# Performance work log

Measured on AMD Instinct MI355X. Metric: run time of the kernel, lower is better.

## Reference

```python
import jax, jax.numpy as jnp
import numpy as np

B, N, K = 4, 8192, 32
HID, INP = 64, 64
IN_CH = HID + INP  # 128; SetConv fc1 sees IN_CH + 3 (relative pos)


def setup_inputs() -> dict:
    key = jax.random.key(0)
    ks = jax.random.split(key, 10)
    return {
        "h": jax.random.normal(ks[0], (B, N, HID), jnp.float32),
        "x": jax.random.normal(ks[1], (B, N, INP), jnp.float32),
        "c": jax.random.normal(ks[2], (B, N, 3), jnp.float32),
        "W1": jax.random.normal(ks[3], (3, IN_CH + 3, HID), jnp.float32) * 0.05,
        "b1": jnp.zeros((3, HID), jnp.float32),
        "W2": jax.random.normal(ks[4], (3, HID, HID), jnp.float32) * 0.05,
        "b2": jnp.zeros((3, HID), jnp.float32),
        "W3": jax.random.normal(ks[5], (3, HID, HID), jnp.float32) * 0.05,
        "b3": jnp.zeros((3, HID), jnp.float32),
        "neigh_idx": jax.random.randint(ks[6], (B, N, K), 0, N, jnp.int32),
        "edge_feats": jax.random.normal(ks[7], (B, N, K, 3), jnp.float32),
    }


def reference(h, x, c, W1, b1, W2, b2, W3, b3, neigh_idx, edge_feats):
    # c (point coordinates) is unused by the GRU body, matching the torch source.
    slope = 0.1

    def setconv(i, feat):
        # gather K neighbor features per point: [B, N, K, C]
        g = jax.vmap(lambda fb, ib: fb[ib])(feat, neigh_idx)
        e = jnp.concatenate([g, edge_feats], axis=-1)  # [B, N, K, C+3]
        y = jax.nn.leaky_relu(jnp.einsum('bnkc,cd->bnkd', e, W1[i]) + b1[i], slope)
        y = y.max(axis=2)  # pool over neighbors -> [B, N, HID]
        y = jax.nn.leaky_relu(y @ W2[i] + b2[i], slope)
        return y @ W3[i] + b3[i]

    hx = jnp.concatenate([h, x], axis=2)
    z = jax.nn.sigmoid(setconv(0, hx))
    r = jax.nn.sigmoid(setconv(1, hx))
    q = jnp.tanh(setconv(2, jnp.concatenate([r * h, x], axis=2)))
    return (1.0 - z) * h + z * q
```

## Files before the change

kernel.cpp:

```cpp
#include <hip/hip_runtime.h>
#include <math.h>

typedef unsigned short u16;
typedef unsigned int u32;
typedef __attribute__((ext_vector_type(8))) short s8v;
typedef __attribute__((ext_vector_type(4))) float f4v;

#define KNBR 32
#define MFMA16(a, b, c) __builtin_amdgcn_mfma_f32_16x16x32_bf16((a), (b), (c), 0, 0, 0)

__device__ __forceinline__ float bf2f(u16 u) { return __uint_as_float((u32)u << 16); }
__device__ __forceinline__ float bflo(u32 u) { return __uint_as_float(u << 16); }
__device__ __forceinline__ float bfhi(u32 u) { return __uint_as_float(u & 0xffff0000u); }
__device__ __forceinline__ u16 f2bf(float f) {
    u32 u = __float_as_uint(f);
    return (u16)((u + 0x7fffu + ((u >> 16) & 1u)) >> 16);
}
__device__ __forceinline__ u32 pk2(float a, float b) {
    return (u32)f2bf(a) | ((u32)f2bf(b) << 16);
}
__device__ __forceinline__ float leaky(float v) { return v >= 0.f ? v : 0.1f * v; }
__device__ __forceinline__ float sigm(float v) { return 1.f / (1.f + expf(-v)); }

__device__ __forceinline__ int swz_plb(int b, int full) {
    if (!full) return b << 6;
    int xcd = b & 7;
    int within = ((b >> 3) << 1) | (xcd & 1);
    return ((xcd >> 1) << 13) + (within << 6);
}

#define T2O 8704
#define T3O 13056
#define T4O 17664
#define T5O 22272
#define T6O 24576
#define TTOT 26880

__global__ __launch_bounds__(512) void k_prep(
    const float* __restrict__ W1f, const float* __restrict__ W2f,
    const float* __restrict__ W3f, u32* __restrict__ TB)
{
    int id = blockIdx.x * 512 + threadIdx.x;
    if (id >= TTOT) return;
    u32 word = 0;
    if (id < T2O) {
        int g = id / 4352, r = id - g * 4352;
        int n = r / 68, kp = r - n * 68;
        if (kp < 64)
            word = pk2(W1f[g * 8384 + kp * 128 + n], W1f[g * 8384 + kp * 128 + 64 + n]);
    } else if (id < T3O) {
        int r = id - T2O;
        int n = r / 68, kp = r - n * 68;
        if (kp < 64)
            word = pk2(W1f[16768 + kp * 128 + n], W1f[16768 + kp * 128 + 64 + n]);
    } else if (id < T4O) {
        int r = id - T3O;
        int g = r / 2304, r2 = r - g * 2304;
        int n = r2 / 36, kp = r2 - n * 36;
        if (kp < 32)
            word = pk2(W2f[g * 4096 + kp * 128 + n], W2f[g * 4096 + kp * 128 + 64 + n]);
    } else if (id < T5O) {
        int r = id - T4O;
        int g = r / 2304, r2 = r - g * 2304;
        int n = r2 / 36, kp = r2 - n * 36;
        if (kp < 32)
            word = pk2(W3f[g * 4096 + kp * 128 + n], W3f[g * 4096 + kp * 128 + 64 + n]);
    } else if (id < T6O) {
        int r = id - T5O;
        int n = r / 36, kp = r - n * 36;
        if (kp < 32)
            word = pk2(W2f[8192 + kp * 128 + n], W2f[8192 + kp * 128 + 64 + n]);
    } else {
        int r = id - T6O;
        int n = r / 36, kp = r - n * 36;
        if (kp < 32)
            word = pk2(W3f[8192 + kp * 128 + n], W3f[8192 + kp * 128 + 64 + n]);
    }
    TB[id] = word;
}


__global__ __launch_bounds__(512) void k_gemm_p01(
    const float* __restrict__ h, const float* __restrict__ x,
    const u32* __restrict__ TB, const float* __restrict__ b1f,
    u32* __restrict__ P01, int p0, int full)
{
    __shared__ u32 a_lds[64 * 68];
    __shared__ u32 wb[8704];
    int t = threadIdx.x;
    int plb = swz_plb(blockIdx.x, full);
    int pgb = p0 + plb;
    for (int i = 0; i < 8; ++i) {
        int id = t + i * 512;
        int p = id >> 6, cw = id & 63;
        const float* src = (cw < 32) ? (h + (size_t)(pgb + p) * 64 + cw * 2)
                                     : (x + (size_t)(pgb + p) * 64 + (cw - 32) * 2);
        float2 v = *(const float2*)src;
        a_lds[p * 68 + cw] = pk2(v.x, v.y);
    }
    for (int i = 0; i < 17; ++i) wb[t + i * 512] = TB[t + i * 512];
    __syncthreads();
    int lane = t & 63;
    int w = __builtin_amdgcn_readfirstlane(t >> 6);
    int m = w & 3, npair = w >> 2;
    int quad = lane >> 4, l15 = lane & 15;
    f4v acc[2][2];
    #pragma unroll
    for (int g = 0; g < 2; ++g)
        #pragma unroll
        for (int nt = 0; nt < 2; ++nt) {
            float b = b1f[g * 64 + (npair * 2 + nt) * 16 + l15];
            acc[g][nt] = (f4v){b, b, b, b};
        }
    #pragma unroll
    for (int kb = 0; kb < 4; ++kb) {
        s8v af = *(const s8v*)&a_lds[(m * 16 + l15) * 68 + kb * 16 + quad * 4];
        #pragma unroll
        for (int g = 0; g < 2; ++g)
            #pragma unroll
            for (int nt = 0; nt < 2; ++nt) {
                s8v bf = *(const s8v*)&wb[(g * 64 + (npair * 2 + nt) * 16 + l15) * 68
                                          + kb * 16 + quad * 4];
                acc[g][nt] = MFMA16(af, bf, acc[g][nt]);
            }
    }
    #pragma unroll
    for (int nt = 0; nt < 2; ++nt)
        #pragma unroll
        for (int r = 0; r < 4; ++r) {
            int pt = m * 16 + quad * 4 + r;
            int ch = (npair * 2 + nt) * 16 + l15;
            P01[(size_t)(plb + pt) * 64 + ch] = pk2(acc[0][nt][r], acc[1][nt][r]);
        }
}

__global__ __launch_bounds__(512) void k_fuse01(
    const u32* __restrict__ P01, const float* __restrict__ W1f,
    const u32* __restrict__ TB,
    const int* __restrict__ nidx, const float* __restrict__ ef,
    const float* __restrict__ h, const float* __restrict__ x,
    const float* __restrict__ b1f, const float* __restrict__ b2f,
    const float* __restrict__ b3f,
    u16* __restrict__ Z, float* __restrict__ P2, int p0, int full)
{
    __shared__ u32 a_lds[64 * 68];
    __shared__ u32 wb[4608];
    __shared__ u32 idx_l[1024];
    __shared__ u32 ef_p[2048];
    __shared__ u32 e2_p[1024];
    int t = threadIdx.x;
    int plb = swz_plb(blockIdx.x, full);
    int pg0 = p0 + plb;
    int rbase = ((pg0 >> 13) << 13) - p0;
    int lane = t & 63;
    int w = __builtin_amdgcn_readfirstlane(t >> 6);
    int quad = lane >> 4, l15 = lane & 15;
    u16* y16 = (u16*)a_lds;

    for (int i = 0; i < 9; ++i) wb[t + i * 512] = TB[T3O + t + i * 512];
    for (int i = 0; i < 2; ++i) {
        int id = t + i * 512;
        int pt = id >> 4, k2 = id & 15;
        int2 nn = *(const int2*)(nidx + (size_t)(pg0 + pt) * KNBR + 2 * k2);
        idx_l[id] = (u32)(rbase + nn.x) | ((u32)(rbase + nn.y) << 16);
        const float* e = ef + ((size_t)(pg0 + pt) * KNBR + 2 * k2) * 3;
        float2 a = *(const float2*)(e);
        float2 b = *(const float2*)(e + 2);
        float2 c = *(const float2*)(e + 4);
        uint2 ev; ev.x = pk2(a.x, a.y); ev.y = pk2(b.y, c.x);
        ((uint2*)ef_p)[id] = ev;
        e2_p[id] = pk2(b.x, c.y);
    }
    __syncthreads();
    {
        float w00 = W1f[8192 + lane], w01 = W1f[8256 + lane], w02 = W1f[8320 + lane];
        float w10 = W1f[16576 + lane], w11 = W1f[16640 + lane], w12 = W1f[16704 + lane];
        const u32* P01l = P01 + lane;
        for (int pp = 0; pp < 8; ++pp) {
            int lp = w * 8 + pp;
            const u32* ib2 = &idx_l[lp * 16];
            const uint2* eb2 = (const uint2*)&ef_p[lp * 32];
            const u32* e2b = &e2_p[lp * 16];
            float m0 = -1e30f, m1 = -1e30f;
            #pragma unroll
            for (int k2 = 0; k2 < 16; ++k2) {
                u32 rw = ib2[k2];
                uint2 ew = eb2[k2];
                u32 e2w = e2b[k2];
                u32 g0 = P01l[(rw & 0xffffu) * 64];
                u32 g1 = P01l[(rw >> 16) * 64];
                float e00 = bflo(ew.x), e01 = bfhi(ew.x), e02 = bflo(e2w);
                float e10 = bflo(ew.y), e11 = bfhi(ew.y), e12 = bfhi(e2w);
                m0 = fmaxf(m0, bflo(g0) + e00 * w00 + e01 * w01 + e02 * w02);
                m1 = fmaxf(m1, bfhi(g0) + e00 * w10 + e01 * w11 + e02 * w12);
                m0 = fmaxf(m0, bflo(g1) + e10 * w00 + e11 * w01 + e12 * w02);
                m1 = fmaxf(m1, bfhi(g1) + e10 * w10 + e11 * w11 + e12 * w12);
            }
            y16[lp * 136 + lane]      = f2bf(leaky(m0));
            y16[lp * 136 + 64 + lane] = f2bf(leaky(m1));
        }
    }
    __syncthreads();
    int m = w & 3, g = w >> 2;
    f4v acc[4];
    #pragma unroll
    for (int nt = 0; nt < 4; ++nt) {
        float b = b2f[g * 64 + nt * 16 + l15];
        acc[nt] = (f4v){b, b, b, b};
    }
    #pragma unroll
    for (int kb = 0; kb < 2; ++kb) {
        s8v af = *(const s8v*)&a_lds[(m * 16 + l15) * 68 + g * 32 + kb * 16 + quad * 4];
        #pragma unroll
        for (int nt = 0; nt < 4; ++nt) {
            s8v bf = *(const s8v*)&wb[(g * 64 + nt * 16 + l15) * 36 + kb * 16 + quad * 4];
            acc[nt] = MFMA16(af, bf, acc[nt]);
        }
    }
    #pragma unroll
    for (int nt = 0; nt < 4; ++nt)
        #pragma unroll
        for (int r = 0; r < 4; ++r)
            y16[(m * 16 + quad * 4 + r) * 136 + g * 64 + nt * 16 + l15] =
                f2bf(leaky(acc[nt][r]));
    __syncthreads();
    for (int i = 0; i < 9; ++i) wb[t + i * 512] = TB[T4O + t + i * 512];
    __syncthreads();
    #pragma unroll
    for (int nt = 0; nt < 4; ++nt) {
        float b = b3f[g * 64 + nt * 16 + l15];
        acc[nt] = (f4v){b, b, b, b};
    }
    #pragma unroll
    for (int kb = 0; kb < 2; ++kb) {
        s8v af = *(const s8v*)&a_lds[(m * 16 + l15) * 68 + g * 32 + kb * 16 + quad * 4];
        #pragma unroll
        for (int nt = 0; nt < 4; ++nt) {
            s8v bf = *(const s8v*)&wb[(g * 64 + nt * 16 + l15) * 36 + kb * 16 + quad * 4];
            acc[nt] = MFMA16(af, bf, acc[nt]);
        }
    }
    __syncthreads();
    if (g == 0) {
        #pragma unroll
        for (int nt = 0; nt < 4; ++nt)
            #pragma unroll
            for (int r = 0; r < 4; ++r) {
                int pt = m * 16 + quad * 4 + r;
                int ch = nt * 16 + l15;
                Z[(size_t)(plb + pt) * 64 + ch] = f2bf(sigm(acc[nt][r]));
            }
    } else {
        #pragma unroll
        for (int nt = 0; nt < 4; ++nt)
            #pragma unroll
            for (int r = 0; r < 4; ++r) {
                int pt = m * 16 + quad * 4 + r;
                int ch = nt * 16 + l15;
                float hv = h[(size_t)(pg0 + pt) * 64 + ch];
                y16[pt * 136 + ch] = f2bf(sigm(acc[nt][r]) * hv);
            }
    }
    for (int i = 0; i < 4; ++i) {
        int id = t + i * 512;
        int p = id >> 5, cw = id & 31;
        float2 v = *(const float2*)(x + (size_t)(pg0 + p) * 64 + cw * 2);
        a_lds[p * 68 + 32 + cw] = pk2(v.x, v.y);
    }
    for (int i = 0; i < 9; ++i) {
        int id = t + i * 512;
        if (id < 4352) wb[id] = TB[T2O + id];
    }
    __syncthreads();
    int nh = w >> 2;
    f4v pacc[2];
    #pragma unroll
    for (int nt = 0; nt < 2; ++nt) {
        float b = b1f[128 + (nh * 2 + nt) * 16 + l15];
        pacc[nt] = (f4v){b, b, b, b};
    }
    #pragma unroll
    for (int kb = 0; kb < 4; ++kb) {
        s8v af = *(const s8v*)&a_lds[(m * 16 + l15) * 68 + kb * 16 + quad * 4];
        #pragma unroll
        for (int nt = 0; nt < 2; ++nt) {
            s8v bf = *(const s8v*)&wb[((nh * 2 + nt) * 16 + l15) * 68 + kb * 16 + quad * 4];
            pacc[nt] = MFMA16(af, bf, pacc[nt]);
        }
    }
    #pragma unroll
    for (int nt = 0; nt < 2; ++nt)
        #pragma unroll
        for (int r = 0; r < 4; ++r) {
            int pt = m * 16 + quad * 4 + r;
            int ch = (nh * 2 + nt) * 16 + l15;
            P2[(size_t)(plb + pt) * 64 + ch] = pacc[nt][r];
        }
}

__global__ __launch_bounds__(512) void k_fuse2(
    const float* __restrict__ P2, const float* __restrict__ W1f,
    const u32* __restrict__ TB,
    const int* __restrict__ nidx, const float* __restrict__ ef,
    const float* __restrict__ b2f, const float* __restrict__ b3f,
    const float* __restrict__ h, const u16* __restrict__ Z,
    float* __restrict__ out, int p0, int full)
{
    __shared__ u32 a_lds[64 * 36];
    __shared__ u32 wb[2304];
    __shared__ u32 idx_l[1024];
    __shared__ u32 ef_p[2048];
    __shared__ u32 e2_p[1024];
    int t = threadIdx.x;
    int plb = swz_plb(blockIdx.x, full);
    int pg0 = p0 + plb;
    int rbase = ((pg0 >> 13) << 13) - p0;
    int lane = t & 63;
    int w = __builtin_amdgcn_readfirstlane(t >> 6);
    int quad = lane >> 4, l15 = lane & 15;
    u16* y16 = (u16*)a_lds;

    for (int i = 0; i < 5; ++i) {
        int id = t + i * 512;
        if (id < 2304) wb[id] = TB[T5O + id];
    }
    for (int i = 0; i < 2; ++i) {
        int id = t + i * 512;
        int pt = id >> 4, k2 = id & 15;
        int2 nn = *(const int2*)(nidx + (size_t)(pg0 + pt) * KNBR + 2 * k2);
        idx_l[id] = (u32)(rbase + nn.x) | ((u32)(rbase + nn.y) << 16);
        const float* e = ef + ((size_t)(pg0 + pt) * KNBR + 2 * k2) * 3;
        float2 a = *(const float2*)(e);
        float2 b = *(const float2*)(e + 2);
        float2 c = *(const float2*)(e + 4);
        uint2 ev; ev.x = pk2(a.x, a.y); ev.y = pk2(b.y, c.x);
        ((uint2*)ef_p)[id] = ev;
        e2_p[id] = pk2(b.x, c.y);
    }
    __syncthreads();
    {
        const float* W = W1f + 2 * 8384;
        float w0 = W[8192 + lane], w1 = W[8256 + lane], w2 = W[8320 + lane];
        const float* P2l = P2 + lane;
        for (int pp = 0; pp < 8; ++pp) {
            int lp = w * 8 + pp;
            const u32* ib2 = &idx_l[lp * 16];
            const uint2* eb2 = (const uint2*)&ef_p[lp * 32];
            const u32* e2b = &e2_p[lp * 16];
            float m = -1e30f;
            #pragma unroll
            for (int k2 = 0; k2 < 16; ++k2) {
                u32 rw = ib2[k2];
                uint2 ew = eb2[k2];
                u32 e2w = e2b[k2];
                float g0 = P2l[(rw & 0xffffu) * 64];
                float g1 = P2l[(rw >> 16) * 64];
                float e00 = bflo(ew.x), e01 = bfhi(ew.x), e02 = bflo(e2w);
                float e10 = bflo(ew.y), e11 = bfhi(ew.y), e12 = bfhi(e2w);
                m = fmaxf(m, g0 + e00 * w0 + e01 * w1 + e02 * w2);
                m = fmaxf(m, g1 + e10 * w0 + e11 * w1 + e12 * w2);
            }
            y16[lp * 72 + lane] = f2bf(leaky(m));
        }
    }
    __syncthreads();
    int m = w & 3, nh = w >> 2;
    f4v acc[2];
    #pragma unroll
    for (int nt = 0; nt < 2; ++nt) {
        float b = b2f[128 + (nh * 2 + nt) * 16 + l15];
        acc[nt] = (f4v){b, b, b, b};
    }
    #pragma unroll
    for (int kb = 0; kb < 2; ++kb) {
        s8v af = *(const s8v*)&a_lds[(m * 16 + l15) * 36 + kb * 16 + quad * 4];
        #pragma unroll
        for (int nt = 0; nt < 2; ++nt) {
            s8v bf = *(const s8v*)&wb[((nh * 2 + nt) * 16 + l15) * 36 + kb * 16 + quad * 4];
            acc[nt] = MFMA16(af, bf, acc[nt]);
        }
    }
    __syncthreads();
    #pragma unroll
    for (int nt = 0; nt < 2; ++nt)
        #pragma unroll
        for (int r = 0; r < 4; ++r)
            y16[(m * 16 + quad * 4 + r) * 72 + (nh * 2 + nt) * 16 + l15] =
                f2bf(leaky(acc[nt][r]));
    for (int i = 0; i < 5; ++i) {
        int id = t + i * 512;
        if (id < 2304) wb[id] = TB[T6O + id];
    }
    __syncthreads();
    #pragma unroll
    for (int nt = 0; nt < 2; ++nt) {
        float b = b3f[128 + (nh * 2 + nt) * 16 + l15];
        acc[nt] = (f4v){b, b, b, b};
    }
    #pragma unroll
    for (int kb = 0; kb < 2; ++kb) {
        s8v af = *(const s8v*)&a_lds[(m * 16 + l15) * 36 + kb * 16 + quad * 4];
        #pragma unroll
        for (int nt = 0; nt < 2; ++nt) {
            s8v bf = *(const s8v*)&wb[((nh * 2 + nt) * 16 + l15) * 36 + kb * 16 + quad * 4];
            acc[nt] = MFMA16(af, bf, acc[nt]);
        }
    }
    #pragma unroll
    for (int nt = 0; nt < 2; ++nt)
        #pragma unroll
        for (int r = 0; r < 4; ++r) {
            int pt = m * 16 + quad * 4 + r;
            int ch = (nh * 2 + nt) * 16 + l15;
            int pl = plb + pt;
            int pg = p0 + pl;
            float z = bf2f(Z[(size_t)pl * 64 + ch]);
            float hv = h[(size_t)pg * 64 + ch];
            out[(size_t)pg * 64 + ch] = (1.f - z) * hv + z * tanhf(acc[nt][r]);
        }
}

extern "C" void kernel_launch(void* const* d_in, const int* in_sizes, int n_in,
                              void* d_out, int out_size, void* d_ws, size_t ws_size,
                              hipStream_t stream)
{
    const float* h  = (const float*)d_in[0];
    const float* x  = (const float*)d_in[1];
    const float* W1 = (const float*)d_in[3];
    const float* b1 = (const float*)d_in[4];
    const float* W2 = (const float*)d_in[5];
    const float* b2 = (const float*)d_in[6];
    const float* W3 = (const float*)d_in[7];
    const float* b3 = (const float*)d_in[8];
    const int* nidx = (const int*)d_in[9];
    const float* ef = (const float*)d_in[10];
    float* out = (float*)d_out;

    char* wsb = (char*)d_ws;
    size_t need_full = 32768ull * 640ull + (size_t)TTOT * 4ull;
    size_t PN = (ws_size >= need_full) ? 32768 : 8192;
    int passes = (int)(32768 / PN);
    int full = (PN == 32768) ? 1 : 0;

    u32* P01  = (u32*)wsb;
    u16* Z    = (u16*)(wsb + PN * 256);
    float* P2 = (float*)(wsb + PN * 384);
    u32* TB   = (u32*)(wsb + PN * 640);

    k_prep<<<dim3((TTOT + 511) / 512), 512, 0, stream>>>(W1, W2, W3, TB);
    for (int s = 0; s < passes; ++s) {
        int p0 = (int)(s * PN);
        dim3 g((unsigned)(PN / 64));
        k_gemm_p01<<<g, 512, 0, stream>>>(h, x, TB, b1, P01, p0, full);
        k_fuse01  <<<g, 512, 0, stream>>>(P01, W1, TB, nidx, ef, h, x,
                                          b1, b2, b3, Z, P2, p0, full);
        k_fuse2   <<<g, 512, 0, stream>>>(P2, W1, TB, nidx, ef,
                                          b2, b3, h, Z, out, p0, full);
    }
}
```

Baseline: 164.3 us.

## Precompute packed edge data once and double block threads to 1024

```diff
diff --git a/kernel.cpp b/kernel.cpp
--- a/kernel.cpp
+++ b/kernel.cpp
@@ -79,8 +79,28 @@
     TB[id] = word;
 }
 
-
-__global__ __launch_bounds__(512) void k_gemm_p01(
+__global__ __launch_bounds__(256) void k_prep_edges(
+    const int* __restrict__ nidx, const float* __restrict__ ef,
+    u32* __restrict__ EP, int p0, int full)
+{
+    int tid = blockIdx.x * 256 + threadIdx.x;
+    int ptl = tid >> 4, k2 = tid & 15;
+    int ptg = p0 + ptl;
+    int2 nn = *(const int2*)(nidx + (size_t)ptg * KNBR + 2 * k2);
+    int rb = full ? ((ptg >> 13) << 13) : 0;
+    u32 idxw = (u32)(rb + nn.x) | ((u32)(rb + nn.y) << 16);
+    const float* e = ef + ((size_t)ptg * KNBR + 2 * k2) * 3;
+    float2 a = *(const float2*)(e);
+    float2 b = *(const float2*)(e + 2);
+    float2 c = *(const float2*)(e + 4);
+    u32* row = EP + (size_t)ptl * 64;
+    row[k2] = idxw;
+    ((uint2*)(row + 16))[k2] = make_uint2(pk2(a.x, a.y), pk2(b.y, c.x));
+    row[48 + k2] = pk2(b.x, c.y);
+}
+
+
+__global__ __launch_bounds__(1024) void k_gemm_p01(
     const float* __restrict__ h, const float* __restrict__ x,
     const u32* __restrict__ TB, const float* __restrict__ b1f,
     u32* __restrict__ P01, int p0, int full)
@@ -90,54 +110,48 @@
     int t = threadIdx.x;
     int plb = swz_plb(blockIdx.x, full);
     int pgb = p0 + plb;
-    for (int i = 0; i < 8; ++i) {
-        int id = t + i * 512;
+    for (int i = 0; i < 4; ++i) {
+        int id = t + i * 1024;
         int p = id >> 6, cw = id & 63;
         const float* src = (cw < 32) ? (h + (size_t)(pgb + p) * 64 + cw * 2)
                                      : (x + (size_t)(pgb + p) * 64 + (cw - 32) * 2);
         float2 v = *(const float2*)src;
         a_lds[p * 68 + cw] = pk2(v.x, v.y);
     }
-    for (int i = 0; i < 17; ++i) wb[t + i * 512] = TB[t + i * 512];
+    for (int i = 0; i < 9; ++i) {
+        int id = t + i * 1024;
+        if (id < 8704) wb[id] = TB[id];
+    }
     __syncthreads();
     int lane = t & 63;
     int w = __builtin_amdgcn_readfirstlane(t >> 6);
-    int m = w & 3, npair = w >> 2;
+    int m = w & 3, nt = w >> 2;
     int quad = lane >> 4, l15 = lane & 15;
-    f4v acc[2][2];
-    #pragma unroll
-    for (int g = 0; g < 2; ++g)
-        #pragma unroll
-        for (int nt = 0; nt < 2; ++nt) {
-            float b = b1f[g * 64 + (npair * 2 + nt) * 16 + l15];
-            acc[g][nt] = (f4v){b, b, b, b};
-        }
+    f4v acc0, acc1;
+    {
+        float b0 = b1f[nt * 16 + l15];
+        float b1 = b1f[64 + nt * 16 + l15];
+        acc0 = (f4v){b0, b0, b0, b0};
+        acc1 = (f4v){b1, b1, b1, b1};
+    }
     #pragma unroll
     for (int kb = 0; kb < 4; ++kb) {
         s8v af = *(const s8v*)&a_lds[(m * 16 + l15) * 68 + kb * 16 + quad * 4];
-        #pragma unroll
-        for (int g = 0; g < 2; ++g)
-            #pragma unroll
-            for (int nt = 0; nt < 2; ++nt) {
-                s8v bf = *(const s8v*)&wb[(g * 64 + (npair * 2 + nt) * 16 + l15) * 68
-                                          + kb * 16 + quad * 4];
-                acc[g][nt] = MFMA16(af, bf, acc[g][nt]);
-            }
-    }
-    #pragma unroll
-    for (int nt = 0; nt < 2; ++nt)
-        #pragma unroll
-        for (int r = 0; r < 4; ++r) {
-            int pt = m * 16 + quad * 4 + r;
-            int ch = (npair * 2 + nt) * 16 + l15;
-            P01[(size_t)(plb + pt) * 64 + ch] = pk2(acc[0][nt][r], acc[1][nt][r]);
-        }
-}
-
-__global__ __launch_bounds__(512) void k_fuse01(
+        s8v bf0 = *(const s8v*)&wb[(nt * 16 + l15) * 68 + kb * 16 + quad * 4];
+        s8v bf1 = *(const s8v*)&wb[(64 + nt * 16 + l15) * 68 + kb * 16 + quad * 4];
+        acc0 = MFMA16(af, bf0, acc0);
+        acc1 = MFMA16(af, bf1, acc1);
+    }
+    #pragma unroll
+    for (int r = 0; r < 4; ++r) {
+        int pt = m * 16 + quad * 4 + r;
+        P01[(size_t)(plb + pt) * 64 + nt * 16 + l15] = pk2(acc0[r], acc1[r]);
+    }
+}
+
+__global__ __launch_bounds__(1024) void k_fuse01(
     const u32* __restrict__ P01, const float* __restrict__ W1f,
-    const u32* __restrict__ TB,
-    const int* __restrict__ nidx, const float* __restrict__ ef,
+    const u32* __restrict__ TB, const u32* __restrict__ EP,
     const float* __restrict__ h, const float* __restrict__ x,
     const float* __restrict__ b1f, const float* __restrict__ b2f,
     const float* __restrict__ b3f,
@@ -145,48 +159,37 @@
 {
     __shared__ u32 a_lds[64 * 68];
     __shared__ u32 wb[4608];
-    __shared__ u32 idx_l[1024];
-    __shared__ u32 ef_p[2048];
-    __shared__ u32 e2_p[1024];
+    __shared__ u32 ep_l[64 * 64];
     int t = threadIdx.x;
     int plb = swz_plb(blockIdx.x, full);
     int pg0 = p0 + plb;
-    int rbase = ((pg0 >> 13) << 13) - p0;
     int lane = t & 63;
     int w = __builtin_amdgcn_readfirstlane(t >> 6);
     int quad = lane >> 4, l15 = lane & 15;
     u16* y16 = (u16*)a_lds;
 
-    for (int i = 0; i < 9; ++i) wb[t + i * 512] = TB[T3O + t + i * 512];
-    for (int i = 0; i < 2; ++i) {
-        int id = t + i * 512;
-        int pt = id >> 4, k2 = id & 15;
-        int2 nn = *(const int2*)(nidx + (size_t)(pg0 + pt) * KNBR + 2 * k2);
-        idx_l[id] = (u32)(rbase + nn.x) | ((u32)(rbase + nn.y) << 16);
-        const float* e = ef + ((size_t)(pg0 + pt) * KNBR + 2 * k2) * 3;
-        float2 a = *(const float2*)(e);
-        float2 b = *(const float2*)(e + 2);
-        float2 c = *(const float2*)(e + 4);
-        uint2 ev; ev.x = pk2(a.x, a.y); ev.y = pk2(b.y, c.x);
-        ((uint2*)ef_p)[id] = ev;
-        e2_p[id] = pk2(b.x, c.y);
+    for (int i = 0; i < 5; ++i) {
+        int id = t + i * 1024;
+        if (id < 4608) wb[id] = TB[T3O + id];
+    }
+    for (int i = 0; i < 4; ++i) {
+        int id = t + i * 1024;
+        ep_l[id] = EP[(size_t)plb * 64 + id];
     }
     __syncthreads();
     {
         float w00 = W1f[8192 + lane], w01 = W1f[8256 + lane], w02 = W1f[8320 + lane];
         float w10 = W1f[16576 + lane], w11 = W1f[16640 + lane], w12 = W1f[16704 + lane];
         const u32* P01l = P01 + lane;
-        for (int pp = 0; pp < 8; ++pp) {
-            int lp = w * 8 + pp;
-            const u32* ib2 = &idx_l[lp * 16];
-            const uint2* eb2 = (const uint2*)&ef_p[lp * 32];
-            const u32* e2b = &e2_p[lp * 16];
+        for (int pp = 0; pp < 4; ++pp) {
+            int lp = w * 4 + pp;
+            const u32* ib = &ep_l[lp * 64];
             float m0 = -1e30f, m1 = -1e30f;
             #pragma unroll
             for (int k2 = 0; k2 < 16; ++k2) {
-                u32 rw = ib2[k2];
-                uint2 ew = eb2[k2];
-                u32 e2w = e2b[k2];
+                u32 rw = ib[k2];
+                uint2 ew = ((const uint2*)(ib + 16))[k2];
+                u32 e2w = ib[48 + k2];
                 u32 g0 = P01l[(rw & 0xffffu) * 64];
                 u32 g1 = P01l[(rw >> 16) * 64];
                 float e00 = bflo(ew.x), e01 = bfhi(ew.x), e02 = bflo(e2w);
@@ -201,158 +204,141 @@
         }
     }
     __syncthreads();
-    int m = w & 3, g = w >> 2;
-    f4v acc[4];
-    #pragma unroll
-    for (int nt = 0; nt < 4; ++nt) {
-        float b = b2f[g * 64 + nt * 16 + l15];
+    int m = w & 3, c = w >> 2, g = c >> 1, np = c & 1;
+    f4v acc[2];
+    #pragma unroll
+    for (int nt = 0; nt < 2; ++nt) {
+        float b = b2f[g * 64 + (np * 2 + nt) * 16 + l15];
         acc[nt] = (f4v){b, b, b, b};
     }
     #pragma unroll
     for (int kb = 0; kb < 2; ++kb) {
         s8v af = *(const s8v*)&a_lds[(m * 16 + l15) * 68 + g * 32 + kb * 16 + quad * 4];
         #pragma unroll
-        for (int nt = 0; nt < 4; ++nt) {
-            s8v bf = *(const s8v*)&wb[(g * 64 + nt * 16 + l15) * 36 + kb * 16 + quad * 4];
+        for (int nt = 0; nt < 2; ++nt) {
+            s8v bf = *(const s8v*)&wb[(g * 64 + (np * 2 + nt) * 16 + l15) * 36
+                                      + kb * 16 + quad * 4];
             acc[nt] = MFMA16(af, bf, acc[nt]);
         }
     }
-    #pragma unroll
-    for (int nt = 0; nt < 4; ++nt)
+    __syncthreads();
+    #pragma unroll
+    for (int nt = 0; nt < 2; ++nt)
         #pragma unroll
         for (int r = 0; r < 4; ++r)
-            y16[(m * 16 + quad * 4 + r) * 136 + g * 64 + nt * 16 + l15] =
+            y16[(m * 16 + quad * 4 + r) * 136 + g * 64 + (np * 2 + nt) * 16 + l15] =
                 f2bf(leaky(acc[nt][r]));
-    __syncthreads();
-    for (int i = 0; i < 9; ++i) wb[t + i * 512] = TB[T4O + t + i * 512];
-    __syncthreads();
-    #pragma unroll
-    for (int nt = 0; nt < 4; ++nt) {
-        float b = b3f[g * 64 + nt * 16 + l15];
+    for (int i = 0; i < 5; ++i) {
+        int id = t + i * 1024;
+        if (id < 4608) wb[id] = TB[T4O + id];
+    }
+    __syncthreads();
+    #pragma unroll
+    for (int nt = 0; nt < 2; ++nt) {
+        float b = b3f[g * 64 + (np * 2 + nt) * 16 + l15];
         acc[nt] = (f4v){b, b, b, b};
     }
     #pragma unroll
     for (int kb = 0; kb < 2; ++kb) {
         s8v af = *(const s8v*)&a_lds[(m * 16 + l15) * 68 + g * 32 + kb * 16 + quad * 4];
         #pragma unroll
-        for (int nt = 0; nt < 4; ++nt) {
-            s8v bf = *(const s8v*)&wb[(g * 64 + nt * 16 + l15) * 36 + kb * 16 + quad * 4];
+        for (int nt = 0; nt < 2; ++nt) {
+            s8v bf = *(const s8v*)&wb[(g * 64 + (np * 2 + nt) * 16 + l15) * 36
+                                      + kb * 16 + quad * 4];
             acc[nt] = MFMA16(af, bf, acc[nt]);
         }
     }
     __syncthreads();
     if (g == 0) {
         #pragma unroll
-        for (int nt = 0; nt < 4; ++nt)
+        for (int nt = 0; nt < 2; ++nt)
             #pragma unroll
             for (int r = 0; r < 4; ++r) {
                 int pt = m * 16 + quad * 4 + r;
-                int ch = nt * 16 + l15;
+                int ch = (np * 2 + nt) * 16 + l15;
                 Z[(size_t)(plb + pt) * 64 + ch] = f2bf(sigm(acc[nt][r]));
             }
     } else {
         #pragma unroll
-        for (int nt = 0; nt < 4; ++nt)
+        for (int nt = 0; nt < 2; ++nt)
             #pragma unroll
             for (int r = 0; r < 4; ++r) {
                 int pt = m * 16 + quad * 4 + r;
-                int ch = nt * 16 + l15;
+                int ch = (np * 2 + nt) * 16 + l15;
                 float hv = h[(size_t)(pg0 + pt) * 64 + ch];
                 y16[pt * 136 + ch] = f2bf(sigm(acc[nt][r]) * hv);
             }
     }
-    for (int i = 0; i < 4; ++i) {
-        int id = t + i * 512;
+    for (int i = 0; i < 2; ++i) {
+        int id = t + i * 1024;
         int p = id >> 5, cw = id & 31;
         float2 v = *(const float2*)(x + (size_t)(pg0 + p) * 64 + cw * 2);
         a_lds[p * 68 + 32 + cw] = pk2(v.x, v.y);
     }
-    for (int i = 0; i < 9; ++i) {
-        int id = t + i * 512;
+    for (int i = 0; i < 5; ++i) {
+        int id = t + i * 1024;
         if (id < 4352) wb[id] = TB[T2O + id];
     }
     __syncthreads();
-    int nh = w >> 2;
-    f4v pacc[2];
-    #pragma unroll
-    for (int nt = 0; nt < 2; ++nt) {
-        float b = b1f[128 + (nh * 2 + nt) * 16 + l15];
-        pacc[nt] = (f4v){b, b, b, b};
+    int n = w >> 2;
+    f4v pacc;
+    {
+        float b = b1f[128 + n * 16 + l15];
+        pacc = (f4v){b, b, b, b};
     }
     #pragma unroll
     for (int kb = 0; kb < 4; ++kb) {
         s8v af = *(const s8v*)&a_lds[(m * 16 + l15) * 68 + kb * 16 + quad * 4];
-        #pragma unroll
-        for (int nt = 0; nt < 2; ++nt) {
-            s8v bf = *(const s8v*)&wb[((nh * 2 + nt) * 16 + l15) * 68 + kb * 16 + quad * 4];
-            pacc[nt] = MFMA16(af, bf, pacc[nt]);
-        }
-    }
-    #pragma unroll
-    for (int nt = 0; nt < 2; ++nt)
-        #pragma unroll
-        for (int r = 0; r < 4; ++r) {
-            int pt = m * 16 + quad * 4 + r;
-            int ch = (nh * 2 + nt) * 16 + l15;
-            P2[(size_t)(plb + pt) * 64 + ch] = pacc[nt][r];
-        }
-}
-
-__global__ __launch_bounds__(512) void k_fuse2(
+        s8v bf = *(const s8v*)&wb[(n * 16 + l15) * 68 + kb * 16 + quad * 4];
+        pacc = MFMA16(af, bf, pacc);
+    }
+    #pragma unroll
+    for (int r = 0; r < 4; ++r) {
+        int pt = m * 16 + quad * 4 + r;
+        P2[(size_t)(plb + pt) * 64 + n * 16 + l15] = pacc[r];
+    }
+}
+
+__global__ __launch_bounds__(1024) void k_fuse2(
     const float* __restrict__ P2, const float* __restrict__ W1f,
-    const u32* __restrict__ TB,
-    const int* __restrict__ nidx, const float* __restrict__ ef,
+    const u32* __restrict__ TB, const u32* __restrict__ EP,
     const float* __restrict__ b2f, const float* __restrict__ b3f,
     const float* __restrict__ h, const u16* __restrict__ Z,
     float* __restrict__ out, int p0, int full)
 {
     __shared__ u32 a_lds[64 * 36];
     __shared__ u32 wb[2304];
-    __shared__ u32 idx_l[1024];
-    __shared__ u32 ef_p[2048];
-    __shared__ u32 e2_p[1024];
+    __shared__ u32 ep_l[64 * 64];
     int t = threadIdx.x;
     int plb = swz_plb(blockIdx.x, full);
     int pg0 = p0 + plb;
-    int rbase = ((pg0 >> 13) << 13) - p0;
     int lane = t & 63;
     int w = __builtin_amdgcn_readfirstlane(t >> 6);
     int quad = lane >> 4, l15 = lane & 15;
     u16* y16 = (u16*)a_lds;
 
-    for (int i = 0; i < 5; ++i) {
-        int id = t + i * 512;
+    for (int i = 0; i < 3; ++i) {
+        int id = t + i * 1024;
         if (id < 2304) wb[id] = TB[T5O + id];
     }
-    for (int i = 0; i < 2; ++i) {
-        int id = t + i * 512;
-        int pt = id >> 4, k2 = id & 15;
-        int2 nn = *(const int2*)(nidx + (size_t)(pg0 + pt) * KNBR + 2 * k2);
-        idx_l[id] = (u32)(rbase + nn.x) | ((u32)(rbase + nn.y) << 16);
-        const float* e = ef + ((size_t)(pg0 + pt) * KNBR + 2 * k2) * 3;
-        float2 a = *(const float2*)(e);
-        float2 b = *(const float2*)(e + 2);
-        float2 c = *(const float2*)(e + 4);
-        uint2 ev; ev.x = pk2(a.x, a.y); ev.y = pk2(b.y, c.x);
-        ((uint2*)ef_p)[id] = ev;
-        e2_p[id] = pk2(b.x, c.y);
+    for (int i = 0; i < 4; ++i) {
+        int id = t + i * 1024;
+        ep_l[id] = EP[(size_t)plb * 64 + id];
     }
     __syncthreads();
     {
         const float* W = W1f + 2 * 8384;
         float w0 = W[8192 + lane], w1 = W[8256 + lane], w2 = W[8320 + lane];
         const float* P2l = P2 + lane;
-        for (int pp = 0; pp < 8; ++pp) {
-            int lp = w * 8 + pp;
-            const u32* ib2 = &idx_l[lp * 16];
-            const uint2* eb2 = (const uint2*)&ef_p[lp * 32];
-            const u32* e2b = &e2_p[lp * 16];
+        for (int pp = 0; pp < 4; ++pp) {
+            int lp = w * 4 + pp;
+            const u32* ib = &ep_l[lp * 64];
             float m = -1e30f;
             #pragma unroll
             for (int k2 = 0; k2 < 16; ++k2) {
-                u32 rw = ib2[k2];
-                uint2 ew = eb2[k2];
-                u32 e2w = e2b[k2];
+                u32 rw = ib[k2];
+                uint2 ew = ((const uint2*)(ib + 16))[k2];
+                u32 e2w = ib[48 + k2];
                 float g0 = P2l[(rw & 0xffffu) * 64];
                 float g1 = P2l[(rw >> 16) * 64];
                 float e00 = bflo(ew.x), e01 = bfhi(ew.x), e02 = bflo(e2w);
@@ -364,60 +350,47 @@
         }
     }
     __syncthreads();
-    int m = w & 3, nh = w >> 2;
-    f4v acc[2];
-    #pragma unroll
-    for (int nt = 0; nt < 2; ++nt) {
-        float b = b2f[128 + (nh * 2 + nt) * 16 + l15];
-        acc[nt] = (f4v){b, b, b, b};
+    int m = w & 3, n = w >> 2;
+    f4v acc;
+    {
+        float b = b2f[128 + n * 16 + l15];
+        acc = (f4v){b, b, b, b};
     }
     #pragma unroll
     for (int kb = 0; kb < 2; ++kb) {
         s8v af = *(const s8v*)&a_lds[(m * 16 + l15) * 36 + kb * 16 + quad * 4];
-        #pragma unroll
-        for (int nt = 0; nt < 2; ++nt) {
-            s8v bf = *(const s8v*)&wb[((nh * 2 + nt) * 16 + l15) * 36 + kb * 16 + quad * 4];
-            acc[nt] = MFMA16(af, bf, acc[nt]);
-        }
-    }
-    __syncthreads();
-    #pragma unroll
-    for (int nt = 0; nt < 2; ++nt)
-        #pragma unroll
-        for (int r = 0; r < 4; ++r)
-            y16[(m * 16 + quad * 4 + r) * 72 + (nh * 2 + nt) * 16 + l15] =
-                f2bf(leaky(acc[nt][r]));
-    for (int i = 0; i < 5; ++i) {
-        int id = t + i * 512;
+        s8v bf = *(const s8v*)&wb[(n * 16 + l15) * 36 + kb * 16 + quad * 4];
+        acc = MFMA16(af, bf, acc);
+    }
+    __syncthreads();
+    #pragma unroll
+    for (int r = 0; r < 4; ++r)
+        y16[(m * 16 + quad * 4 + r) * 72 + n * 16 + l15] = f2bf(leaky(acc[r]));
+    for (int i = 0; i < 3; ++i) {
+        int id = t + i * 1024;
         if (id < 2304) wb[id] = TB[T6O + id];
     }
     __syncthreads();
-    #pragma unroll
-    for (int nt = 0; nt < 2; ++nt) {
-        float b = b3f[128 + (nh * 2 + nt) * 16 + l15];
-        acc[nt] = (f4v){b, b, b, b};
+    {
+        float b = b3f[128 + n * 16 + l15];
+        acc = (f4v){b, b, b, b};
     }
     #pragma unroll
     for (int kb = 0; kb < 2; ++kb) {
         s8v af = *(const s8v*)&a_lds[(m * 16 + l15) * 36 + kb * 16 + quad * 4];
-        #pragma unroll
-        for (int nt = 0; nt < 2; ++nt) {
-            s8v bf = *(const s8v*)&wb[((nh * 2 + nt) * 16 + l15) * 36 + kb * 16 + quad * 4];
-            acc[nt] = MFMA16(af, bf, acc[nt]);
-        }
-    }
-    #pragma unroll
-    for (int nt = 0; nt < 2; ++nt)
-        #pragma unroll
-        for (int r = 0; r < 4; ++r) {
-            int pt = m * 16 + quad * 4 + r;
-            int ch = (nh * 2 + nt) * 16 + l15;
-            int pl = plb + pt;
-            int pg = p0 + pl;
-            float z = bf2f(Z[(size_t)pl * 64 + ch]);
-            float hv = h[(size_t)pg * 64 + ch];
-            out[(size_t)pg * 64 + ch] = (1.f - z) * hv + z * tanhf(acc[nt][r]);
-        }
+        s8v bf = *(const s8v*)&wb[(n * 16 + l15) * 36 + kb * 16 + quad * 4];
+        acc = MFMA16(af, bf, acc);
+    }
+    #pragma unroll
+    for (int r = 0; r < 4; ++r) {
+        int pt = m * 16 + quad * 4 + r;
+        int ch = n * 16 + l15;
+        int pl = plb + pt;
+        int pg = p0 + pl;
+        float z = bf2f(Z[(size_t)pl * 64 + ch]);
+        float hv = h[(size_t)pg * 64 + ch];
+        out[(size_t)pg * 64 + ch] = (1.f - z) * hv + z * tanhf(acc[r]);
+    }
 }
 
 extern "C" void kernel_launch(void* const* d_in, const int* in_sizes, int n_in,
@@ -437,7 +410,7 @@
     float* out = (float*)d_out;
 
     char* wsb = (char*)d_ws;
-    size_t need_full = 32768ull * 640ull + (size_t)TTOT * 4ull;
+    size_t need_full = 32768ull * 896ull + (size_t)TTOT * 4ull;
     size_t PN = (ws_size >= need_full) ? 32768 : 8192;
     int passes = (int)(32768 / PN);
     int full = (PN == 32768) ? 1 : 0;
@@ -445,16 +418,18 @@
     u32* P01  = (u32*)wsb;
     u16* Z    = (u16*)(wsb + PN * 256);
     float* P2 = (float*)(wsb + PN * 384);
-    u32* TB   = (u32*)(wsb + PN * 640);
+    u32* EP   = (u32*)(wsb + PN * 640);
+    u32* TB   = (u32*)(wsb + PN * 896);
 
     k_prep<<<dim3((TTOT + 511) / 512), 512, 0, stream>>>(W1, W2, W3, TB);
     for (int s = 0; s < passes; ++s) {
         int p0 = (int)(s * PN);
         dim3 g((unsigned)(PN / 64));
-        k_gemm_p01<<<g, 512, 0, stream>>>(h, x, TB, b1, P01, p0, full);
-        k_fuse01  <<<g, 512, 0, stream>>>(P01, W1, TB, nidx, ef, h, x,
-                                          b1, b2, b3, Z, P2, p0, full);
-        k_fuse2   <<<g, 512, 0, stream>>>(P2, W1, TB, nidx, ef,
-                                          b2, b3, h, Z, out, p0, full);
-    }
-}
+        k_prep_edges<<<dim3((unsigned)(PN * 16 / 256)), 256, 0, stream>>>(nidx, ef, EP, p0, full);
+        k_gemm_p01<<<g, 1024, 0, stream>>>(h, x, TB, b1, P01, p0, full);
+        k_fuse01  <<<g, 1024, 0, stream>>>(P01, W1, TB, EP, h, x,
+                                           b1, b2, b3, Z, P2, p0, full);
+        k_fuse2   <<<g, 1024, 0, stream>>>(P2, W1, TB, EP,
+                                           b2, b3, h, Z, out, p0, full);
+    }
+}
```

Measured after the change: 165.4 us. About the same (+0.7%).
